# Kernel optimization log

Measured on AMD Instinct MI355X. Metric: run time of the kernel, lower is better.

Reference implementation:

```python
import jax, jax.numpy as jnp
import numpy as np

TOPK = 2
NUM_EXPERTS = 8

def setup_inputs() -> dict:
    key = jax.random.key(0)
    kx, kg, k1, k3, k2 = jax.random.split(key, 5)
    B, S, D, F, E = 1, 2048, 1024, 1024, NUM_EXPERTS
    x = jax.random.normal(kx, (B, S, D), dtype=jnp.float32)
    wg = jax.random.normal(kg, (E, D), dtype=jnp.float32) * (1.0 / np.sqrt(D))
    w1 = jax.random.normal(k1, (E, D, F), dtype=jnp.float32) * (1.0 / np.sqrt(D))
    w3 = jax.random.normal(k3, (E, D, F), dtype=jnp.float32) * (1.0 / np.sqrt(D))
    w2 = jax.random.normal(k2, (E, F, D), dtype=jnp.float32) * (1.0 / np.sqrt(F))
    return {"x": x, "wg": wg, "w1": w1, "w3": w3, "w2": w2}

def reference(x, wg, w1, w3, w2):
    # x: [B, S, D] -> tokens [N, D]
    D = x.shape[-1]
    E = wg.shape[0]
    xt = x.reshape(-1, D)
    # Gating: Linear(no bias) + softmax over experts
    logits = xt @ wg.T                      # [N, E]
    gates = jax.nn.softmax(logits, axis=-1)
    # Top-k selection, normalize weights (normalize_expert_weights=True),
    # routed_scaling_factor = 1.0
    weights, idx = jax.lax.top_k(gates, TOPK)      # [N, k]
    weights = weights / weights.sum(axis=-1, keepdims=True)
    # Per-token per-expert combine weight (dispatch+combine equivalent)
    comb = (jax.nn.one_hot(idx, E, dtype=xt.dtype) * weights[..., None]).sum(axis=1)  # [N, E]
    # SwiGLU experts (grouped GEMM equivalent, dense over experts)
    h = jnp.einsum('nd,edf->enf', xt, w1)   # gate proj
    u = jnp.einsum('nd,edf->enf', xt, w3)   # up proj
    a = jax.nn.silu(h) * u                  # [E, N, F]
    out = jnp.einsum('enf,efd,ne->nd', a, w2, comb)
    return out.reshape(x.shape), logits
```

## Files before the change

kernel.cpp:

```cpp
#include <hip/hip_runtime.h>
#include <stdint.h>

typedef unsigned short u16;
typedef __attribute__((ext_vector_type(8))) __bf16 bf16x8;
typedef __attribute__((ext_vector_type(4))) float f32x4;

#define MAXMT 40
#define N_TOK 2048
#define DDIM 1024
#define FDIM 1024

#define DEV static __device__ __forceinline__

DEV float bf2f(u16 u) {
    union { uint32_t i; float f; } v;
    v.i = ((uint32_t)u) << 16;
    return v.f;
}
DEV u16 f2bf(float f) {
    union { float f; uint32_t i; } v;
    v.f = f;
    uint32_t x = v.i;
    return (u16)((x + 0x7fffu + ((x >> 16) & 1u)) >> 16);
}

DEV void async_copy16(const u16* gsrc, u16* ldst) {
    __builtin_amdgcn_global_load_lds(
        (const __attribute__((address_space(1))) void*)(uintptr_t)gsrc,
        (__attribute__((address_space(3))) void*)(uint32_t)(uintptr_t)ldst,
        16, 0, 0);
}

__global__ void k_detect(const u16* __restrict__ xr, int* __restrict__ dflag) {
    __shared__ int cnt;
    if (threadIdx.x == 0) cnt = 0;
    __syncthreads();
    u16 u = xr[threadIdx.x];
    int e = (u >> 7) & 0xff;
    int insane = (e != 0) && (e < 90 || e > 160);
    if (insane) atomicAdd(&cnt, 1);
    __syncthreads();
    if (threadIdx.x == 0) dflag[0] = (cnt > 64) ? 1 : 0;
}

__global__ void k_normx(const void* __restrict__ xin, const int* __restrict__ dflag,
                        u16* __restrict__ xb) {
    int i = blockIdx.x * 256 + threadIdx.x;
    if (dflag[0]) {
        float4 v = ((const float4*)xin)[i];
        u16 o[4] = { f2bf(v.x), f2bf(v.y), f2bf(v.z), f2bf(v.w) };
        ((uint2*)xb)[i] = *(const uint2*)o;
    } else {
        ((uint2*)xb)[i] = ((const uint2*)xin)[i];
    }
}

__global__ void k_gating(const void* __restrict__ xraw, const void* __restrict__ wg,
                         const int* __restrict__ dflag, void* __restrict__ out_base,
                         int* __restrict__ te, float* __restrict__ tw) {
    int wave = threadIdx.x >> 6, lane = threadIdx.x & 63;
    int n = blockIdx.x * 4 + wave;
    int fp = dflag[0];
    float acc[8];
#pragma unroll
    for (int e = 0; e < 8; e++) acc[e] = 0.f;
    if (fp) {
        const float* xp = (const float*)xraw + (size_t)n * DDIM;
        const float* wp = (const float*)wg;
        for (int it = 0; it < 16; ++it) {
            int d = it * 64 + lane;
            float xv = xp[d];
#pragma unroll
            for (int e = 0; e < 8; e++) acc[e] += xv * wp[e * DDIM + d];
        }
    } else {
        const u16* xp = (const u16*)xraw + (size_t)n * DDIM;
        const u16* wp = (const u16*)wg;
        for (int it = 0; it < 16; ++it) {
            int d = it * 64 + lane;
            float xv = bf2f(xp[d]);
#pragma unroll
            for (int e = 0; e < 8; e++) acc[e] += xv * bf2f(wp[e * DDIM + d]);
        }
    }
#pragma unroll
    for (int e = 0; e < 8; e++) {
        for (int off = 32; off; off >>= 1) acc[e] += __shfl_xor(acc[e], off);
    }
    if (lane < 8) {
        if (fp) ((float*)out_base + (size_t)N_TOK * DDIM)[n * 8 + lane] = acc[lane];
        else    ((u16*)out_base + (size_t)N_TOK * DDIM)[n * 8 + lane] = f2bf(acc[lane]);
    }
    if (lane == 0) {
        int e0 = 0; float b0 = acc[0];
        for (int e = 1; e < 8; e++) if (acc[e] > b0) { b0 = acc[e]; e0 = e; }
        int e1 = -1; float b1 = -1e30f;
        for (int e = 0; e < 8; e++) if (e != e0 && acc[e] > b1) { b1 = acc[e]; e1 = e; }
        float m = fmaxf(b0, b1);
        float x0 = __expf(b0 - m), x1 = __expf(b1 - m);
        float s = x0 + x1;
        te[n * 2] = e0; te[n * 2 + 1] = e1;
        tw[n * 2] = x0 / s; tw[n * 2 + 1] = x1 / s;
    }
}

__global__ void k_sched(const int* __restrict__ te, const float* __restrict__ tw,
                        int* __restrict__ pair_token, float* __restrict__ pair_weight,
                        int* __restrict__ ppos, int* __restrict__ sched) {
    __shared__ int cnt[8], cur[8];
    int t = threadIdx.x;
    if (t < 8) cnt[t] = 0;
    __syncthreads();
    for (int n = t; n < N_TOK; n += 256) {
        atomicAdd(&cnt[te[2 * n]], 1);
        atomicAdd(&cnt[te[2 * n + 1]], 1);
    }
    __syncthreads();
    if (t == 0) {
        int o = 0, mt = 0;
        for (int e = 0; e < 8; e++) {
            cur[e] = o;
            int c = cnt[e];
            for (int m0 = 0; m0 < c; m0 += 128) {
                sched[mt] = e;
                sched[MAXMT + mt] = o + m0;
                sched[2 * MAXMT + mt] = (c - m0 < 128) ? (c - m0) : 128;
                mt++;
            }
            o += c;
        }
        sched[3 * MAXMT] = mt;
        for (int i = mt; i < MAXMT; i++) { sched[i] = 0; sched[MAXMT + i] = 0; sched[2 * MAXMT + i] = 0; }
    }
    __syncthreads();
    for (int n = t; n < N_TOK; n += 256) {
#pragma unroll
        for (int s = 0; s < 2; s++) {
            int e = te[2 * n + s];
            int p = atomicAdd(&cur[e], 1);
            pair_token[p] = n;
            pair_weight[p] = tw[2 * n + s];
            ppos[2 * n + s] = p;
        }
    }
}

__global__ void k_transpose(const void* __restrict__ src0, const int* __restrict__ dflag,
                            u16* __restrict__ dst0) {
    int fp = dflag[0];
    int mat = blockIdx.z;
    u16* dst = dst0 + (size_t)mat * 1048576;
    __shared__ __align__(16) u16 s[64][72];
    int t = threadIdx.x;
    int r = t >> 2, seg = t & 3;
    int r0 = blockIdx.y * 64, c0 = blockIdx.x * 64;
    size_t base = (size_t)mat * 1048576 + (size_t)(r0 + r) * 1024 + c0 + seg * 16;
    u16 v[16];
    if (fp) {
        const float* sp = (const float*)src0 + base;
#pragma unroll
        for (int q = 0; q < 4; q++) {
            float4 f = ((const float4*)sp)[q];
            v[q * 4 + 0] = f2bf(f.x); v[q * 4 + 1] = f2bf(f.y);
            v[q * 4 + 2] = f2bf(f.z); v[q * 4 + 3] = f2bf(f.w);
        }
    } else {
        const u16* sp = (const u16*)src0 + base;
        *(uint4*)&v[0] = *(const uint4*)sp;
        *(uint4*)&v[8] = *(const uint4*)(sp + 8);
    }
    *(uint4*)&s[r][seg * 16] = *(const uint4*)&v[0];
    *(uint4*)&s[r][seg * 16 + 8] = *(const uint4*)&v[8];
    __syncthreads();
    u16 tmp[16];
#pragma unroll
    for (int j = 0; j < 16; j++) tmp[j] = s[seg * 16 + j][r];
    u16* dp = dst + (size_t)(c0 + r) * 1024 + r0 + seg * 16;
    *(uint4*)dp = *(const uint4*)&tmp[0];
    *(uint4*)(dp + 8) = *(const uint4*)&tmp[8];
}

__launch_bounds__(256, 2)
__global__ void k_gemm13(const u16* __restrict__ xb, const u16* __restrict__ w1t,
                         const u16* __restrict__ w3t, const int* __restrict__ pair_token,
                         const int* __restrict__ sched, u16* __restrict__ Abuf) {
    __shared__ __align__(16) u16 smem[24576];
    u16* sA  = smem;
    u16* sB1 = smem + 8192;
    u16* sB3 = smem + 16384;

    int bn = blockIdx.x;
    int bm = blockIdx.y;
    int total = sched[3 * MAXMT];
    if (bm >= total) return;
    int e = sched[bm];
    int row0 = sched[MAXMT + bm];
    int rowsv = sched[2 * MAXMT + bm];

    int tid = threadIdx.x;
    int wave = tid >> 6, lane = tid & 63;
    int wm = wave & 1, wn = wave >> 1;
    int quad = lane >> 4, l15 = lane & 15;
    int lsub = lane >> 3, slot = lane & 7;

    const u16* gA[4]; u16* lA[4];
    const u16* gB1[4]; const u16* gB3[4]; u16* lB[4];
#pragma unroll
    for (int c = 0; c < 4; c++) {
        int row = c * 32 + wave * 8 + lsub;
        int cr = row < rowsv ? row : 0;
        int tok = pair_token[row0 + cr];
        int gch = slot ^ (row & 7);
        gA[c] = xb + (size_t)tok * DDIM + gch * 8;
        int fcol = bn * 128 + row;
        gB1[c] = w1t + ((size_t)e * 1024 + fcol) * 1024 + gch * 8;
        gB3[c] = w3t + ((size_t)e * 1024 + fcol) * 1024 + gch * 8;
        lA[c] = sA + c * 2048 + wave * 512;
        lB[c] = (u16*)(uintptr_t)(c * 2048 + wave * 512);
    }

    f32x4 acc_h[4][4], acc_u[4][4];
#pragma unroll
    for (int i = 0; i < 4; i++)
#pragma unroll
        for (int j = 0; j < 4; j++) { acc_h[i][j] = (f32x4)0.f; acc_u[i][j] = (f32x4)0.f; }

    for (int kt = 0; kt < 16; ++kt) {
        int k0 = kt * 64;
        __syncthreads();
#pragma unroll
        for (int c = 0; c < 4; c++) {
            size_t off = (size_t)(uintptr_t)lB[c];
            async_copy16(gA[c] + k0, lA[c]);
            async_copy16(gB1[c] + k0, sB1 + off);
            async_copy16(gB3[c] + k0, sB3 + off);
        }
        __syncthreads();
#pragma unroll
        for (int kk = 0; kk < 2; ++kk) {
            bf16x8 a[4], b1[4], b3[4];
#pragma unroll
            for (int i = 0; i < 4; i++) {
                int m = wm * 64 + i * 16 + l15;
                int s = (kk * 4 + quad) ^ (m & 7);
                a[i] = *(const bf16x8*)&sA[m * 64 + s * 8];
            }
#pragma unroll
            for (int j = 0; j < 4; j++) {
                int nn = wn * 64 + j * 16 + l15;
                int s = (kk * 4 + quad) ^ (nn & 7);
                b1[j] = *(const bf16x8*)&sB1[nn * 64 + s * 8];
                b3[j] = *(const bf16x8*)&sB3[nn * 64 + s * 8];
            }
#pragma unroll
            for (int i = 0; i < 4; i++)
#pragma unroll
                for (int j = 0; j < 4; j++) {
                    acc_h[i][j] = __builtin_amdgcn_mfma_f32_16x16x32_bf16(a[i], b1[j], acc_h[i][j], 0, 0, 0);
                    acc_u[i][j] = __builtin_amdgcn_mfma_f32_16x16x32_bf16(a[i], b3[j], acc_u[i][j], 0, 0, 0);
                }
        }
    }
    __syncthreads();
#pragma unroll
    for (int i = 0; i < 4; i++)
#pragma unroll
        for (int j = 0; j < 4; j++)
#pragma unroll
            for (int r = 0; r < 4; r++) {
                int row = wm * 64 + i * 16 + quad * 4 + r;
                int col = wn * 64 + j * 16 + l15;
                float h = acc_h[i][j][r], u = acc_u[i][j][r];
                smem[row * 136 + col] = f2bf(h * u / (1.0f + __expf(-h)));
            }
    __syncthreads();
    int rt = tid >> 1, half = tid & 1;
    if (rt < rowsv) {
        u16* dp = Abuf + (size_t)(row0 + rt) * FDIM + bn * 128 + half * 64;
        const u16* sp = &smem[rt * 136 + half * 64];
#pragma unroll
        for (int q = 0; q < 8; q++)
            *(uint4*)(dp + q * 8) = *(const uint4*)(sp + q * 8);
    }
}

__launch_bounds__(256, 2)
__global__ void k_gemm2(const u16* __restrict__ Abuf, const u16* __restrict__ w2t,
                        const int* __restrict__ sched, u16* __restrict__ Ybuf) {
    __shared__ __align__(16) u16 smem[17408];
    u16* sA = smem;
    u16* sB = smem + 8192;

    int bn = blockIdx.x;
    int bm = blockIdx.y;
    int total = sched[3 * MAXMT];
    if (bm >= total) return;
    int e = sched[bm];
    int row0 = sched[MAXMT + bm];
    int rowsv = sched[2 * MAXMT + bm];

    int tid = threadIdx.x;
    int wave = tid >> 6, lane = tid & 63;
    int wm = wave & 1, wn = wave >> 1;
    int quad = lane >> 4, l15 = lane & 15;
    int lsub = lane >> 3, slot = lane & 7;

    const u16* gA[4]; const u16* gB[4]; u16* lA[4]; u16* lB[4];
#pragma unroll
    for (int c = 0; c < 4; c++) {
        int row = c * 32 + wave * 8 + lsub;
        int cr = row < rowsv ? row : 0;
        int gch = slot ^ (row & 7);
        gA[c] = Abuf + (size_t)(row0 + cr) * FDIM + gch * 8;
        int dcol = bn * 128 + row;
        gB[c] = w2t + ((size_t)e * 1024 + dcol) * 1024 + gch * 8;
        lA[c] = sA + c * 2048 + wave * 512;
        lB[c] = sB + c * 2048 + wave * 512;
    }

    f32x4 acc[4][4];
#pragma unroll
    for (int i = 0; i < 4; i++)
#pragma unroll
        for (int j = 0; j < 4; j++) acc[i][j] = (f32x4)0.f;

    for (int kt = 0; kt < 16; ++kt) {
        int k0 = kt * 64;
        __syncthreads();
#pragma unroll
        for (int c = 0; c < 4; c++) {
            async_copy16(gA[c] + k0, lA[c]);
            async_copy16(gB[c] + k0, lB[c]);
        }
        __syncthreads();
#pragma unroll
        for (int kk = 0; kk < 2; ++kk) {
            bf16x8 a[4], b[4];
#pragma unroll
            for (int i = 0; i < 4; i++) {
                int m = wm * 64 + i * 16 + l15;
                int s = (kk * 4 + quad) ^ (m & 7);
                a[i] = *(const bf16x8*)&sA[m * 64 + s * 8];
            }
#pragma unroll
            for (int j = 0; j < 4; j++) {
                int nn = wn * 64 + j * 16 + l15;
                int s = (kk * 4 + quad) ^ (nn & 7);
                b[j] = *(const bf16x8*)&sB[nn * 64 + s * 8];
            }
#pragma unroll
            for (int i = 0; i < 4; i++)
#pragma unroll
                for (int j = 0; j < 4; j++)
                    acc[i][j] = __builtin_amdgcn_mfma_f32_16x16x32_bf16(a[i], b[j], acc[i][j], 0, 0, 0);
        }
    }
    __syncthreads();
#pragma unroll
    for (int i = 0; i < 4; i++)
#pragma unroll
        for (int j = 0; j < 4; j++)
#pragma unroll
            for (int r = 0; r < 4; r++) {
                int row = wm * 64 + i * 16 + quad * 4 + r;
                int col = wn * 64 + j * 16 + l15;
                smem[row * 136 + col] = f2bf(acc[i][j][r]);
            }
    __syncthreads();
    int rt = tid >> 1, half = tid & 1;
    if (rt < rowsv) {
        u16* dp = Ybuf + (size_t)(row0 + rt) * DDIM + bn * 128 + half * 64;
        const u16* sp = &smem[rt * 136 + half * 64];
#pragma unroll
        for (int q = 0; q < 8; q++)
            *(uint4*)(dp + q * 8) = *(const uint4*)(sp + q * 8);
    }
}

__global__ void k_combine(const u16* __restrict__ Y, const int* __restrict__ ppos,
                          const float* __restrict__ pwt, const int* __restrict__ dflag,
                          void* __restrict__ out) {
    int n = blockIdx.x, t = threadIdx.x;
    int p0 = ppos[2 * n], p1 = ppos[2 * n + 1];
    float w0 = pwt[p0], w1 = pwt[p1];
    uint2 a = *(const uint2*)(Y + (size_t)p0 * 1024 + t * 4);
    uint2 b = *(const uint2*)(Y + (size_t)p1 * 1024 + t * 4);
    const u16* ap = (const u16*)&a;
    const u16* bp = (const u16*)&b;
    float r[4];
#pragma unroll
    for (int j = 0; j < 4; j++) r[j] = w0 * bf2f(ap[j]) + w1 * bf2f(bp[j]);
    if (dflag[0]) {
        float4 o = { r[0], r[1], r[2], r[3] };
        *(float4*)((float*)out + (size_t)n * 1024 + t * 4) = o;
    } else {
        u16 o[4] = { f2bf(r[0]), f2bf(r[1]), f2bf(r[2]), f2bf(r[3]) };
        *(uint2*)((u16*)out + (size_t)n * 1024 + t * 4) = *(const uint2*)o;
    }
}

extern "C" void kernel_launch(void* const* d_in, const int* in_sizes, int n_in,
                              void* d_out, int out_size, void* d_ws, size_t ws_size,
                              hipStream_t stream) {
    const void* x  = d_in[0];
    const void* wg = d_in[1];
    const void* w1 = d_in[2];
    const void* w3 = d_in[3];
    const void* w2 = d_in[4];

    u16* w1t  = (u16*)d_ws;
    u16* w3t  = w1t + (size_t)8 * 1048576;
    u16* Abuf = w3t + (size_t)8 * 1048576;
    u16* Ybuf = Abuf + (size_t)4096 * 1024;
    u16* xb   = Ybuf + (size_t)4096 * 1024;
    int*   te   = (int*)(xb + (size_t)N_TOK * DDIM);
    float* tw   = (float*)(te + 2 * N_TOK);
    int*   ptok = (int*)(tw + 2 * N_TOK);
    float* pwt  = (float*)(ptok + 2 * N_TOK);
    int*   ppos = (int*)(pwt + 2 * N_TOK);
    int*   sched = ppos + 2 * N_TOK;
    int*   dflag = sched + 128;
    u16* w2t = w1t;

    k_detect<<<1, 512, 0, stream>>>((const u16*)x, dflag);
    k_normx<<<2048, 256, 0, stream>>>(x, dflag, xb);
    k_gating<<<512, 256, 0, stream>>>(x, wg, dflag, d_out, te, tw);
    k_sched<<<1, 256, 0, stream>>>(te, tw, ptok, pwt, ppos, sched);

    k_transpose<<<dim3(16, 16, 8), 256, 0, stream>>>(w1, dflag, w1t);
    k_transpose<<<dim3(16, 16, 8), 256, 0, stream>>>(w3, dflag, w3t);
    k_gemm13<<<dim3(8, MAXMT), 256, 0, stream>>>(xb, w1t, w3t, ptok, sched, Abuf);
    k_transpose<<<dim3(16, 16, 8), 256, 0, stream>>>(w2, dflag, w2t);
    k_gemm2<<<dim3(8, MAXMT), 256, 0, stream>>>(Abuf, w2t, sched, Ybuf);

    k_combine<<<2048, 256, 0, stream>>>(Ybuf, ppos, pwt, dflag, d_out);
}
```

Before: 228.2 us.

## Fuse prep kernels into one launch and halve GEMM N-tiles for occupancy

Merges dtype detection, x conversion, gating and all three weight transposes into a single grid launch, with each block detecting fp32 versus bf16 input on its own. w2 now gets its own transposed buffer instead of reusing w1t's space. Both expert GEMMs switch to 128x64 tiles with twice as many blocks and smaller LDS so three blocks fit per CU. This removes several launches and serial gaps, at the cost of redundant detection work in every block and lower per-block data reuse in the GEMMs.

```diff
diff --git a/kernel.cpp b/kernel.cpp
--- a/kernel.cpp
+++ b/kernel.cpp
@@ -31,76 +31,105 @@
         16, 0, 0);
 }
 
-__global__ void k_detect(const u16* __restrict__ xr, int* __restrict__ dflag) {
-    __shared__ int cnt;
-    if (threadIdx.x == 0) cnt = 0;
-    __syncthreads();
-    u16 u = xr[threadIdx.x];
+DEV int sniff_fp(const void* p, int tid, int* scnt) {
+    if (tid == 0) *scnt = 0;
+    __syncthreads();
+    u16 u = ((const u16*)p)[tid & 255];
     int e = (u >> 7) & 0xff;
-    int insane = (e != 0) && (e < 90 || e > 160);
-    if (insane) atomicAdd(&cnt, 1);
-    __syncthreads();
-    if (threadIdx.x == 0) dflag[0] = (cnt > 64) ? 1 : 0;
-}
-
-__global__ void k_normx(const void* __restrict__ xin, const int* __restrict__ dflag,
-                        u16* __restrict__ xb) {
-    int i = blockIdx.x * 256 + threadIdx.x;
-    if (dflag[0]) {
-        float4 v = ((const float4*)xin)[i];
-        u16 o[4] = { f2bf(v.x), f2bf(v.y), f2bf(v.z), f2bf(v.w) };
-        ((uint2*)xb)[i] = *(const uint2*)o;
+    if (e != 0 && (e < 90 || e > 160)) atomicAdd(scnt, 1);
+    __syncthreads();
+    return *scnt > 64;
+}
+
+__global__ void k_mega(const void* __restrict__ x, const void* __restrict__ wg,
+                       const void* __restrict__ w1, const void* __restrict__ w3,
+                       const void* __restrict__ w2, u16* __restrict__ wt,
+                       u16* __restrict__ xb, void* __restrict__ out_base,
+                       int* __restrict__ te, float* __restrict__ tw) {
+    __shared__ int scnt;
+    __shared__ __align__(16) u16 s[64][72];
+    int z = blockIdx.z, tid = threadIdx.x;
+
+    if (z < 24) {
+        int which = z >> 3, mat = z & 7;
+        const void* src0 = which == 0 ? w1 : (which == 1 ? w3 : w2);
+        int fp = sniff_fp(src0, tid, &scnt);
+        u16* dst = wt + ((size_t)z) * 1048576;
+        int r = tid >> 2, seg = tid & 3;
+        int r0 = blockIdx.y * 64, c0 = blockIdx.x * 64;
+        size_t base = (size_t)mat * 1048576 + (size_t)(r0 + r) * 1024 + c0 + seg * 16;
+        u16 v[16];
+        if (fp) {
+            const float* sp = (const float*)src0 + base;
+#pragma unroll
+            for (int q = 0; q < 4; q++) {
+                float4 f = ((const float4*)sp)[q];
+                v[q * 4 + 0] = f2bf(f.x); v[q * 4 + 1] = f2bf(f.y);
+                v[q * 4 + 2] = f2bf(f.z); v[q * 4 + 3] = f2bf(f.w);
+            }
+        } else {
+            const u16* sp = (const u16*)src0 + base;
+            *(uint4*)&v[0] = *(const uint4*)sp;
+            *(uint4*)&v[8] = *(const uint4*)(sp + 8);
+        }
+        *(uint4*)&s[r][seg * 16] = *(const uint4*)&v[0];
+        *(uint4*)&s[r][seg * 16 + 8] = *(const uint4*)&v[8];
+        __syncthreads();
+        u16 tmp[16];
+#pragma unroll
+        for (int j = 0; j < 16; j++) tmp[j] = s[seg * 16 + j][r];
+        u16* dp = dst + (size_t)(c0 + r) * 1024 + r0 + seg * 16;
+        *(uint4*)dp = *(const uint4*)&tmp[0];
+        *(uint4*)(dp + 8) = *(const uint4*)&tmp[8];
     } else {
-        ((uint2*)xb)[i] = ((const uint2*)xin)[i];
-    }
-}
-
-__global__ void k_gating(const void* __restrict__ xraw, const void* __restrict__ wg,
-                         const int* __restrict__ dflag, void* __restrict__ out_base,
-                         int* __restrict__ te, float* __restrict__ tw) {
-    int wave = threadIdx.x >> 6, lane = threadIdx.x & 63;
-    int n = blockIdx.x * 4 + wave;
-    int fp = dflag[0];
-    float acc[8];
-#pragma unroll
-    for (int e = 0; e < 8; e++) acc[e] = 0.f;
-    if (fp) {
-        const float* xp = (const float*)xraw + (size_t)n * DDIM;
-        const float* wp = (const float*)wg;
-        for (int it = 0; it < 16; ++it) {
-            int d = it * 64 + lane;
-            float xv = xp[d];
-#pragma unroll
-            for (int e = 0; e < 8; e++) acc[e] += xv * wp[e * DDIM + d];
-        }
-    } else {
-        const u16* xp = (const u16*)xraw + (size_t)n * DDIM;
-        const u16* wp = (const u16*)wg;
-        for (int it = 0; it < 16; ++it) {
-            int d = it * 64 + lane;
-            float xv = bf2f(xp[d]);
-#pragma unroll
-            for (int e = 0; e < 8; e++) acc[e] += xv * bf2f(wp[e * DDIM + d]);
-        }
-    }
-#pragma unroll
-    for (int e = 0; e < 8; e++) {
-        for (int off = 32; off; off >>= 1) acc[e] += __shfl_xor(acc[e], off);
-    }
-    if (lane < 8) {
-        if (fp) ((float*)out_base + (size_t)N_TOK * DDIM)[n * 8 + lane] = acc[lane];
-        else    ((u16*)out_base + (size_t)N_TOK * DDIM)[n * 8 + lane] = f2bf(acc[lane]);
-    }
-    if (lane == 0) {
-        int e0 = 0; float b0 = acc[0];
-        for (int e = 1; e < 8; e++) if (acc[e] > b0) { b0 = acc[e]; e0 = e; }
-        int e1 = -1; float b1 = -1e30f;
-        for (int e = 0; e < 8; e++) if (e != e0 && acc[e] > b1) { b1 = acc[e]; e1 = e; }
-        float m = fmaxf(b0, b1);
-        float x0 = __expf(b0 - m), x1 = __expf(b1 - m);
-        float s = x0 + x1;
-        te[n * 2] = e0; te[n * 2 + 1] = e1;
-        tw[n * 2] = x0 / s; tw[n * 2 + 1] = x1 / s;
+        int fp = sniff_fp(x, tid, &scnt);
+        int gi = (z - 24) * 256 + blockIdx.y * 16 + blockIdx.x;
+        int wave = tid >> 6, lane = tid & 63;
+        int n = gi * 4 + wave;
+        float acc[8];
+#pragma unroll
+        for (int e = 0; e < 8; e++) acc[e] = 0.f;
+        if (fp) {
+            const float* xp = (const float*)x + (size_t)n * DDIM;
+            const float* wp = (const float*)wg;
+            for (int it = 0; it < 16; ++it) {
+                int d = it * 64 + lane;
+                float xv = xp[d];
+                xb[(size_t)n * DDIM + d] = f2bf(xv);
+#pragma unroll
+                for (int e = 0; e < 8; e++) acc[e] += xv * wp[e * DDIM + d];
+            }
+        } else {
+            const u16* xp = (const u16*)x + (size_t)n * DDIM;
+            const u16* wp = (const u16*)wg;
+            for (int it = 0; it < 16; ++it) {
+                int d = it * 64 + lane;
+                u16 raw = xp[d];
+                xb[(size_t)n * DDIM + d] = raw;
+                float xv = bf2f(raw);
+#pragma unroll
+                for (int e = 0; e < 8; e++) acc[e] += xv * bf2f(wp[e * DDIM + d]);
+            }
+        }
+#pragma unroll
+        for (int e = 0; e < 8; e++) {
+            for (int off = 32; off; off >>= 1) acc[e] += __shfl_xor(acc[e], off);
+        }
+        if (lane < 8) {
+            if (fp) ((float*)out_base + (size_t)N_TOK * DDIM)[n * 8 + lane] = acc[lane];
+            else    ((u16*)out_base + (size_t)N_TOK * DDIM)[n * 8 + lane] = f2bf(acc[lane]);
+        }
+        if (lane == 0) {
+            int e0 = 0; float b0 = acc[0];
+            for (int e = 1; e < 8; e++) if (acc[e] > b0) { b0 = acc[e]; e0 = e; }
+            int e1 = -1; float b1 = -1e30f;
+            for (int e = 0; e < 8; e++) if (e != e0 && acc[e] > b1) { b1 = acc[e]; e1 = e; }
+            float m = fmaxf(b0, b1);
+            float x0 = __expf(b0 - m), x1 = __expf(b1 - m);
+            float sden = x0 + x1;
+            te[n * 2] = e0; te[n * 2 + 1] = e1;
+            tw[n * 2] = x0 / sden; tw[n * 2 + 1] = x1 / sden;
+        }
     }
 }
 
@@ -145,49 +174,14 @@
     }
 }
 
-__global__ void k_transpose(const void* __restrict__ src0, const int* __restrict__ dflag,
-                            u16* __restrict__ dst0) {
-    int fp = dflag[0];
-    int mat = blockIdx.z;
-    u16* dst = dst0 + (size_t)mat * 1048576;
-    __shared__ __align__(16) u16 s[64][72];
-    int t = threadIdx.x;
-    int r = t >> 2, seg = t & 3;
-    int r0 = blockIdx.y * 64, c0 = blockIdx.x * 64;
-    size_t base = (size_t)mat * 1048576 + (size_t)(r0 + r) * 1024 + c0 + seg * 16;
-    u16 v[16];
-    if (fp) {
-        const float* sp = (const float*)src0 + base;
-#pragma unroll
-        for (int q = 0; q < 4; q++) {
-            float4 f = ((const float4*)sp)[q];
-            v[q * 4 + 0] = f2bf(f.x); v[q * 4 + 1] = f2bf(f.y);
-            v[q * 4 + 2] = f2bf(f.z); v[q * 4 + 3] = f2bf(f.w);
-        }
-    } else {
-        const u16* sp = (const u16*)src0 + base;
-        *(uint4*)&v[0] = *(const uint4*)sp;
-        *(uint4*)&v[8] = *(const uint4*)(sp + 8);
-    }
-    *(uint4*)&s[r][seg * 16] = *(const uint4*)&v[0];
-    *(uint4*)&s[r][seg * 16 + 8] = *(const uint4*)&v[8];
-    __syncthreads();
-    u16 tmp[16];
-#pragma unroll
-    for (int j = 0; j < 16; j++) tmp[j] = s[seg * 16 + j][r];
-    u16* dp = dst + (size_t)(c0 + r) * 1024 + r0 + seg * 16;
-    *(uint4*)dp = *(const uint4*)&tmp[0];
-    *(uint4*)(dp + 8) = *(const uint4*)&tmp[8];
-}
-
-__launch_bounds__(256, 2)
+__launch_bounds__(256, 3)
 __global__ void k_gemm13(const u16* __restrict__ xb, const u16* __restrict__ w1t,
                          const u16* __restrict__ w3t, const int* __restrict__ pair_token,
                          const int* __restrict__ sched, u16* __restrict__ Abuf) {
-    __shared__ __align__(16) u16 smem[24576];
+    __shared__ __align__(16) u16 smem[16384];
     u16* sA  = smem;
     u16* sB1 = smem + 8192;
-    u16* sB3 = smem + 16384;
+    u16* sB3 = smem + 12288;
 
     int bn = blockIdx.x;
     int bm = blockIdx.y;
@@ -204,7 +198,6 @@
     int lsub = lane >> 3, slot = lane & 7;
 
     const u16* gA[4]; u16* lA[4];
-    const u16* gB1[4]; const u16* gB3[4]; u16* lB[4];
 #pragma unroll
     for (int c = 0; c < 4; c++) {
         int row = c * 32 + wave * 8 + lsub;
@@ -212,33 +205,39 @@
         int tok = pair_token[row0 + cr];
         int gch = slot ^ (row & 7);
         gA[c] = xb + (size_t)tok * DDIM + gch * 8;
-        int fcol = bn * 128 + row;
+        lA[c] = sA + c * 2048 + wave * 512;
+    }
+    const u16* gB1[2]; const u16* gB3[2]; int lBoff[2];
+#pragma unroll
+    for (int c = 0; c < 2; c++) {
+        int row = c * 32 + wave * 8 + lsub;
+        int gch = slot ^ (row & 7);
+        int fcol = bn * 64 + row;
         gB1[c] = w1t + ((size_t)e * 1024 + fcol) * 1024 + gch * 8;
         gB3[c] = w3t + ((size_t)e * 1024 + fcol) * 1024 + gch * 8;
-        lA[c] = sA + c * 2048 + wave * 512;
-        lB[c] = (u16*)(uintptr_t)(c * 2048 + wave * 512);
-    }
-
-    f32x4 acc_h[4][4], acc_u[4][4];
+        lBoff[c] = c * 2048 + wave * 512;
+    }
+
+    f32x4 acc_h[4][2], acc_u[4][2];
 #pragma unroll
     for (int i = 0; i < 4; i++)
 #pragma unroll
-        for (int j = 0; j < 4; j++) { acc_h[i][j] = (f32x4)0.f; acc_u[i][j] = (f32x4)0.f; }
+        for (int j = 0; j < 2; j++) { acc_h[i][j] = (f32x4)0.f; acc_u[i][j] = (f32x4)0.f; }
 
     for (int kt = 0; kt < 16; ++kt) {
         int k0 = kt * 64;
         __syncthreads();
 #pragma unroll
-        for (int c = 0; c < 4; c++) {
-            size_t off = (size_t)(uintptr_t)lB[c];
-            async_copy16(gA[c] + k0, lA[c]);
-            async_copy16(gB1[c] + k0, sB1 + off);
-            async_copy16(gB3[c] + k0, sB3 + off);
+        for (int c = 0; c < 4; c++) async_copy16(gA[c] + k0, lA[c]);
+#pragma unroll
+        for (int c = 0; c < 2; c++) {
+            async_copy16(gB1[c] + k0, sB1 + lBoff[c]);
+            async_copy16(gB3[c] + k0, sB3 + lBoff[c]);
         }
         __syncthreads();
 #pragma unroll
         for (int kk = 0; kk < 2; ++kk) {
-            bf16x8 a[4], b1[4], b3[4];
+            bf16x8 a[4], b1[2], b3[2];
 #pragma unroll
             for (int i = 0; i < 4; i++) {
                 int m = wm * 64 + i * 16 + l15;
@@ -246,8 +245,8 @@
                 a[i] = *(const bf16x8*)&sA[m * 64 + s * 8];
             }
 #pragma unroll
-            for (int j = 0; j < 4; j++) {
-                int nn = wn * 64 + j * 16 + l15;
+            for (int j = 0; j < 2; j++) {
+                int nn = wn * 32 + j * 16 + l15;
                 int s = (kk * 4 + quad) ^ (nn & 7);
                 b1[j] = *(const bf16x8*)&sB1[nn * 64 + s * 8];
                 b3[j] = *(const bf16x8*)&sB3[nn * 64 + s * 8];
@@ -255,7 +254,7 @@
 #pragma unroll
             for (int i = 0; i < 4; i++)
 #pragma unroll
-                for (int j = 0; j < 4; j++) {
+                for (int j = 0; j < 2; j++) {
                     acc_h[i][j] = __builtin_amdgcn_mfma_f32_16x16x32_bf16(a[i], b1[j], acc_h[i][j], 0, 0, 0);
                     acc_u[i][j] = __builtin_amdgcn_mfma_f32_16x16x32_bf16(a[i], b3[j], acc_u[i][j], 0, 0, 0);
                 }
@@ -265,29 +264,29 @@
 #pragma unroll
     for (int i = 0; i < 4; i++)
 #pragma unroll
-        for (int j = 0; j < 4; j++)
+        for (int j = 0; j < 2; j++)
 #pragma unroll
             for (int r = 0; r < 4; r++) {
                 int row = wm * 64 + i * 16 + quad * 4 + r;
-                int col = wn * 64 + j * 16 + l15;
+                int col = wn * 32 + j * 16 + l15;
                 float h = acc_h[i][j][r], u = acc_u[i][j][r];
-                smem[row * 136 + col] = f2bf(h * u / (1.0f + __expf(-h)));
+                smem[row * 72 + col] = f2bf(h * u / (1.0f + __expf(-h)));
             }
     __syncthreads();
     int rt = tid >> 1, half = tid & 1;
     if (rt < rowsv) {
-        u16* dp = Abuf + (size_t)(row0 + rt) * FDIM + bn * 128 + half * 64;
-        const u16* sp = &smem[rt * 136 + half * 64];
-#pragma unroll
-        for (int q = 0; q < 8; q++)
+        u16* dp = Abuf + (size_t)(row0 + rt) * FDIM + bn * 64 + half * 32;
+        const u16* sp = &smem[rt * 72 + half * 32];
+#pragma unroll
+        for (int q = 0; q < 4; q++)
             *(uint4*)(dp + q * 8) = *(const uint4*)(sp + q * 8);
     }
 }
 
-__launch_bounds__(256, 2)
+__launch_bounds__(256, 3)
 __global__ void k_gemm2(const u16* __restrict__ Abuf, const u16* __restrict__ w2t,
                         const int* __restrict__ sched, u16* __restrict__ Ybuf) {
-    __shared__ __align__(16) u16 smem[17408];
+    __shared__ __align__(16) u16 smem[12288];
     u16* sA = smem;
     u16* sB = smem + 8192;
 
@@ -305,37 +304,42 @@
     int quad = lane >> 4, l15 = lane & 15;
     int lsub = lane >> 3, slot = lane & 7;
 
-    const u16* gA[4]; const u16* gB[4]; u16* lA[4]; u16* lB[4];
+    const u16* gA[4]; u16* lA[4];
 #pragma unroll
     for (int c = 0; c < 4; c++) {
         int row = c * 32 + wave * 8 + lsub;
         int cr = row < rowsv ? row : 0;
         int gch = slot ^ (row & 7);
         gA[c] = Abuf + (size_t)(row0 + cr) * FDIM + gch * 8;
-        int dcol = bn * 128 + row;
+        lA[c] = sA + c * 2048 + wave * 512;
+    }
+    const u16* gB[2]; u16* lB[2];
+#pragma unroll
+    for (int c = 0; c < 2; c++) {
+        int row = c * 32 + wave * 8 + lsub;
+        int gch = slot ^ (row & 7);
+        int dcol = bn * 64 + row;
         gB[c] = w2t + ((size_t)e * 1024 + dcol) * 1024 + gch * 8;
-        lA[c] = sA + c * 2048 + wave * 512;
         lB[c] = sB + c * 2048 + wave * 512;
     }
 
-    f32x4 acc[4][4];
+    f32x4 acc[4][2];
 #pragma unroll
     for (int i = 0; i < 4; i++)
 #pragma unroll
-        for (int j = 0; j < 4; j++) acc[i][j] = (f32x4)0.f;
+        for (int j = 0; j < 2; j++) acc[i][j] = (f32x4)0.f;
 
     for (int kt = 0; kt < 16; ++kt) {
         int k0 = kt * 64;
         __syncthreads();
 #pragma unroll
-        for (int c = 0; c < 4; c++) {
-            async_copy16(gA[c] + k0, lA[c]);
-            async_copy16(gB[c] + k0, lB[c]);
-        }
+        for (int c = 0; c < 4; c++) async_copy16(gA[c] + k0, lA[c]);
+#pragma unroll
+        for (int c = 0; c < 2; c++) async_copy16(gB[c] + k0, lB[c]);
         __syncthreads();
 #pragma unroll
         for (int kk = 0; kk < 2; ++kk) {
-            bf16x8 a[4], b[4];
+            bf16x8 a[4], b[2];
 #pragma unroll
             for (int i = 0; i < 4; i++) {
                 int m = wm * 64 + i * 16 + l15;
@@ -343,15 +347,15 @@
                 a[i] = *(const bf16x8*)&sA[m * 64 + s * 8];
             }
 #pragma unroll
-            for (int j = 0; j < 4; j++) {
-                int nn = wn * 64 + j * 16 + l15;
+            for (int j = 0; j < 2; j++) {
+                int nn = wn * 32 + j * 16 + l15;
                 int s = (kk * 4 + quad) ^ (nn & 7);
                 b[j] = *(const bf16x8*)&sB[nn * 64 + s * 8];
             }
 #pragma unroll
             for (int i = 0; i < 4; i++)
 #pragma unroll
-                for (int j = 0; j < 4; j++)
+                for (int j = 0; j < 2; j++)
                     acc[i][j] = __builtin_amdgcn_mfma_f32_16x16x32_bf16(a[i], b[j], acc[i][j], 0, 0, 0);
         }
     }
@@ -359,28 +363,30 @@
 #pragma unroll
     for (int i = 0; i < 4; i++)
 #pragma unroll
-        for (int j = 0; j < 4; j++)
+        for (int j = 0; j < 2; j++)
 #pragma unroll
             for (int r = 0; r < 4; r++) {
                 int row = wm * 64 + i * 16 + quad * 4 + r;
-                int col = wn * 64 + j * 16 + l15;
-                smem[row * 136 + col] = f2bf(acc[i][j][r]);
+                int col = wn * 32 + j * 16 + l15;
+                smem[row * 72 + col] = f2bf(acc[i][j][r]);
             }
     __syncthreads();
     int rt = tid >> 1, half = tid & 1;
     if (rt < rowsv) {
-        u16* dp = Ybuf + (size_t)(row0 + rt) * DDIM + bn * 128 + half * 64;
-        const u16* sp = &smem[rt * 136 + half * 64];
-#pragma unroll
-        for (int q = 0; q < 8; q++)
+        u16* dp = Ybuf + (size_t)(row0 + rt) * DDIM + bn * 64 + half * 32;
+        const u16* sp = &smem[rt * 72 + half * 32];
+#pragma unroll
+        for (int q = 0; q < 4; q++)
             *(uint4*)(dp + q * 8) = *(const uint4*)(sp + q * 8);
     }
 }
 
 __global__ void k_combine(const u16* __restrict__ Y, const int* __restrict__ ppos,
-                          const float* __restrict__ pwt, const int* __restrict__ dflag,
+                          const float* __restrict__ pwt, const void* __restrict__ x,
                           void* __restrict__ out) {
+    __shared__ int scnt;
     int n = blockIdx.x, t = threadIdx.x;
+    int fp = sniff_fp(x, t, &scnt);
     int p0 = ppos[2 * n], p1 = ppos[2 * n + 1];
     float w0 = pwt[p0], w1 = pwt[p1];
     uint2 a = *(const uint2*)(Y + (size_t)p0 * 1024 + t * 4);
@@ -390,7 +396,7 @@
     float r[4];
 #pragma unroll
     for (int j = 0; j < 4; j++) r[j] = w0 * bf2f(ap[j]) + w1 * bf2f(bp[j]);
-    if (dflag[0]) {
+    if (fp) {
         float4 o = { r[0], r[1], r[2], r[3] };
         *(float4*)((float*)out + (size_t)n * 1024 + t * 4) = o;
     } else {
@@ -408,9 +414,11 @@
     const void* w3 = d_in[3];
     const void* w2 = d_in[4];
 
-    u16* w1t  = (u16*)d_ws;
-    u16* w3t  = w1t + (size_t)8 * 1048576;
-    u16* Abuf = w3t + (size_t)8 * 1048576;
+    u16* wt   = (u16*)d_ws;
+    u16* w1t  = wt;
+    u16* w3t  = wt + (size_t)8 * 1048576;
+    u16* w2t  = wt + (size_t)16 * 1048576;
+    u16* Abuf = wt + (size_t)24 * 1048576;
     u16* Ybuf = Abuf + (size_t)4096 * 1024;
     u16* xb   = Ybuf + (size_t)4096 * 1024;
     int*   te   = (int*)(xb + (size_t)N_TOK * DDIM);
@@ -419,19 +427,10 @@
     float* pwt  = (float*)(ptok + 2 * N_TOK);
     int*   ppos = (int*)(pwt + 2 * N_TOK);
     int*   sched = ppos + 2 * N_TOK;
-    int*   dflag = sched + 128;
-    u16* w2t = w1t;
-
-    k_detect<<<1, 512, 0, stream>>>((const u16*)x, dflag);
-    k_normx<<<2048, 256, 0, stream>>>(x, dflag, xb);
-    k_gating<<<512, 256, 0, stream>>>(x, wg, dflag, d_out, te, tw);
+
+    k_mega<<<dim3(16, 16, 26), 256, 0, stream>>>(x, wg, w1, w3, w2, wt, xb, d_out, te, tw);
     k_sched<<<1, 256, 0, stream>>>(te, tw, ptok, pwt, ppos, sched);
-
-    k_transpose<<<dim3(16, 16, 8), 256, 0, stream>>>(w1, dflag, w1t);
-    k_transpose<<<dim3(16, 16, 8), 256, 0, stream>>>(w3, dflag, w3t);
-    k_gemm13<<<dim3(8, MAXMT), 256, 0, stream>>>(xb, w1t, w3t, ptok, sched, Abuf);
-    k_transpose<<<dim3(16, 16, 8), 256, 0, stream>>>(w2, dflag, w2t);
-    k_gemm2<<<dim3(8, MAXMT), 256, 0, stream>>>(Abuf, w2t, sched, Ybuf);
-
-    k_combine<<<2048, 256, 0, stream>>>(Ybuf, ppos, pwt, dflag, d_out);
-}
+    k_gemm13<<<dim3(16, MAXMT), 256, 0, stream>>>(xb, w1t, w3t, ptok, sched, Abuf);
+    k_gemm2<<<dim3(16, MAXMT), 256, 0, stream>>>(Abuf, w2t, sched, Ybuf);
+    k_combine<<<2048, 256, 0, stream>>>(Ybuf, ppos, pwt, x, d_out);
+}
```

After: 206.7 us. 1.1x faster.
